# Performance work log

Hardware: AMD Instinct MI355X
Metric: run time of the kernel (lower is better)

The kernel has to match this reference:

```python
import jax, jax.numpy as jnp
import numpy as np

B, T, D, S = 64, 577, 768, 577  # batch, seq, hidden, v-out (=seq of e)


def setup_inputs() -> dict:
    key = jax.random.key(0)
    ks = jax.random.split(key, 8)
    sc = 1.0 / np.sqrt(D)
    return {
        "b": jax.random.normal(ks[0], (B, T, D), jnp.float32),
        "e": jax.random.normal(ks[1], (B, T, D), jnp.float32),
        "Wq": jax.random.normal(ks[2], (D, D), jnp.float32) * sc,
        "bq": jnp.zeros((D,), jnp.float32),
        "Wk": jax.random.normal(ks[3], (D, D), jnp.float32) * sc,
        "bk": jnp.zeros((D,), jnp.float32),
        "Wv": jax.random.normal(ks[4], (S, D), jnp.float32) * sc,
        "bv": jnp.zeros((S,), jnp.float32),
    }


def reference(b, e, Wq, bq, Wk, bk, Wv, bv):
    # Dropout layers are identity in eval mode.
    q = b @ Wq.T + bq                      # [B,T,D]
    k = e @ Wk.T + bk                      # [B,S,D]
    v = b @ Wv.T + bv                      # [B,T,S]
    # tanh(Q K^T) @ V^T : [B,T,S] @ [B,S,T] -> [B,T,T]
    attn = jnp.tanh(jnp.einsum("btd,bsd->bts", q, k))
    out = jnp.einsum("bts,bus->btu", attn, v)
    return out  # squeeze is a no-op for B>1
```

## Files before the change

### kernel.cpp

```cpp
#include <hip/hip_runtime.h>
#include <hip/hip_fp16.h>


typedef _Float16 f16x8 __attribute__((ext_vector_type(8)));
typedef _Float16 f16x4 __attribute__((ext_vector_type(4)));
typedef float f32x4 __attribute__((ext_vector_type(4)));

__global__ void cvt8_kernel(const float* __restrict__ src, _Float16* __restrict__ dst,
                            long long n8) {
    long long i = blockIdx.x * (long long)blockDim.x + threadIdx.x;
    const long long stride = gridDim.x * (long long)blockDim.x;
    for (; i < n8; i += stride) {
        const float4 f0 = ((const float4*)src)[2 * i];
        const float4 f1 = ((const float4*)src)[2 * i + 1];
        f16x8 h;
        h[0] = (_Float16)f0.x; h[1] = (_Float16)f0.y; h[2] = (_Float16)f0.z; h[3] = (_Float16)f0.w;
        h[4] = (_Float16)f1.x; h[5] = (_Float16)f1.y; h[6] = (_Float16)f1.z; h[7] = (_Float16)f1.w;
        ((f16x8*)dst)[i] = h;
    }
}

__global__ void cvtT_kernel(const float* __restrict__ src, _Float16* __restrict__ dst) {
    __shared__ float t[32][33];
    const int bx = blockIdx.x, by = blockIdx.y;
    const int tx = threadIdx.x & 31, ty = threadIdx.x >> 5;
#pragma unroll
    for (int k = 0; k < 4; ++k) {
        const int r = ty + 8 * k;
        t[r][tx] = src[(size_t)(by * 32 + r) * 768 + bx * 32 + tx];
    }
    __syncthreads();
#pragma unroll
    for (int k = 0; k < 4; ++k) {
        const int r = ty + 8 * k;
        dst[(size_t)(bx * 32 + r) * 768 + by * 32 + tx] = (_Float16)t[tx][r];
    }
}

__global__ void prep_kernel(const _Float16* __restrict__ WqT, const _Float16* __restrict__ WkT,
                            const float* __restrict__ bq, const float* __restrict__ bk,
                            float* __restrict__ w2f, _Float16* __restrict__ Mt_aug,
                            float* __restrict__ bias_aug) {
    const int wid = blockIdx.x * 4 + (threadIdx.x >> 6);
    const int lane = threadIdx.x & 63;
    if (wid < 768) {
        float s = 0.f;
        for (int k = 0; k < 12; ++k) s += (float)WqT[(size_t)wid * 768 + lane + 64 * k] * bk[lane + 64 * k];
        for (int o = 32; o; o >>= 1) s += __shfl_xor(s, o);
        if (lane == 0) Mt_aug[(size_t)768 * 768 + wid] = (_Float16)s;
    } else if (wid < 1536) {
        const int n = wid - 768;
        float s = 0.f;
        for (int k = 0; k < 12; ++k) s += (float)WkT[(size_t)n * 768 + lane + 64 * k] * bq[lane + 64 * k];
        for (int o = 32; o; o >>= 1) s += __shfl_xor(s, o);
        if (lane == 0) w2f[n] = s;
    } else if (wid == 1536) {
        float s = 0.f;
        for (int k = 0; k < 12; ++k) s += bq[lane + 64 * k] * bk[lane + 64 * k];
        for (int o = 32; o; o >>= 1) s += __shfl_xor(s, o);
        for (int k = 0; k < 12; ++k) bias_aug[lane + 64 * k] = 0.f;
        if (lane < 32) {
            float v = 0.f;
            if (lane == 0) v = s;
            if (lane == 1) v = 1.f;
            bias_aug[768 + lane] = v;
        }
    } else if (wid < 1568) {
        const int r = 769 + (wid - 1537);
        if (r < 800)
            for (int k = 0; k < 12; ++k) Mt_aug[(size_t)r * 768 + lane + 64 * k] = (_Float16)0.f;
    }
}

__global__ void cvt_e_aug_kernel(const float* __restrict__ e, const float* __restrict__ w2f,
                                 _Float16* __restrict__ dst, int rows) {
    const int wpb = blockDim.x >> 6;
    int wid = blockIdx.x * wpb + (threadIdx.x >> 6);
    const int nw = gridDim.x * wpb;
    const int lane = threadIdx.x & 63;
    for (int s = wid; s < rows; s += nw) {
        const float4* er = (const float4*)(e + (size_t)s * 768);
        _Float16* dr = dst + (size_t)s * 800;
        float dot = 0.f;
#pragma unroll
        for (int k = 0; k < 3; ++k) {
            const int idx = lane + 64 * k;
            const float4 v = er[idx];
            const float4 w = ((const float4*)w2f)[idx];
            dot += v.x * w.x + v.y * w.y + v.z * w.z + v.w * w.w;
            f16x4 h;
            h[0] = (_Float16)v.x; h[1] = (_Float16)v.y;
            h[2] = (_Float16)v.z; h[3] = (_Float16)v.w;
            *(f16x4*)(dr + 4 * idx) = h;
        }
        for (int o = 32; o; o >>= 1) dot += __shfl_xor(dot, o);
        if (lane < 32) {
            _Float16 v = (_Float16)0.f;
            if (lane == 0) v = (_Float16)1.f;
            if (lane == 1) v = (_Float16)dot;
            dr[768 + lane] = v;
        }
    }
}

__device__ __forceinline__ void gload16(const _Float16* g, _Float16* l) {
    __builtin_amdgcn_global_load_lds(
        (const __attribute__((address_space(1))) unsigned int*)(g),
        (__attribute__((address_space(3))) unsigned int*)(l),
        16, 0, 0);
}

template<bool TANH, bool OUT_F16, bool BIAS, int MODE>
__global__ __launch_bounds__(256)
void gemm_nt_f16(const _Float16* __restrict__ A, const _Float16* __restrict__ Bt,
                 const float* __restrict__ bias, void* __restrict__ Cp,
                 int M, int Nreal, int Nstore, int K,
                 int lda, int ldb, int ldc, int nTileN, int nTiles,
                 long long sA, long long sB, long long sC)
{
    __shared__ __align__(16) _Float16 lds[3 * 8192];

    int bid = blockIdx.x;
    int z, tm, tn;
    if (MODE == 0) {
        const int nwg = gridDim.x;
        const int q8 = nwg >> 3, r8 = nwg & 7;
        const int xcd = bid & 7, loc = bid >> 3;
        bid = (xcd < r8 ? xcd * (q8 + 1) : r8 * (q8 + 1) + (xcd - r8) * q8) + loc;
        z = 0;
        tm = bid / nTileN; tn = bid - tm * nTileN;
    } else {
        const int xcd = bid & 7, idx = bid >> 3;
        const int g = idx / nTiles, tile = idx - g * nTiles;
        z = g * 8 + xcd;
        tm = tile / nTileN; tn = tile - tm * nTileN;
    }
    const int m0 = tm << 7, n0 = tn << 7;

    const _Float16* Az = A + (size_t)z * sA;
    const _Float16* Bz = Bt + (size_t)z * sB;

    const int tid = threadIdx.x;
    const int lane = tid & 63;
    const int wid = tid >> 6;
    const int wm = wid >> 1, wn = wid & 1;

    const int r0 = tid >> 2;
    const int c0 = (((tid & 3) ^ ((tid >> 3) & 3)) << 3);
    const int rA0 = (m0 + r0      < M ? m0 + r0      : M - 1);
    const int rA1 = (m0 + r0 + 64 < M ? m0 + r0 + 64 : M - 1);
    const int rB0 = (n0 + r0      < Nreal ? n0 + r0      : Nreal - 1);
    const int rB1 = (n0 + r0 + 64 < Nreal ? n0 + r0 + 64 : Nreal - 1);
    const _Float16* pA0 = Az + (size_t)rA0 * lda + c0;
    const _Float16* pA1 = Az + (size_t)rA1 * lda + c0;
    const _Float16* pB0 = Bz + (size_t)rB0 * ldb + c0;
    const _Float16* pB1 = Bz + (size_t)rB1 * ldb + c0;

    const int o0 = tid * 8, o1 = (tid + 256) * 8;

    const int rr = lane & 15;
    const int hh = lane >> 4;
    const int sw = (rr >> 1) & 3;
    const int fAo = ((wm * 64 + rr) * 4 + (hh ^ sw)) * 8;
    const int fBo = ((wn * 64 + rr) * 4 + (hh ^ sw)) * 8;

    const f32x4 z4 = {0.f, 0.f, 0.f, 0.f};
    f32x4 acc[4][4];
#pragma unroll
    for (int i = 0; i < 4; ++i)
#pragma unroll
        for (int j = 0; j < 4; ++j) acc[i][j] = z4;

    const int nt = K >> 5;

#define STAGE(si, kt)                                              \
    do {                                                           \
        _Float16* base_ = lds + (si) * 8192;                       \
        const int ko_ = (kt) << 5;                                 \
        gload16(pA0 + ko_, base_ + o0);                            \
        gload16(pA1 + ko_, base_ + o1);                            \
        gload16(pB0 + ko_, base_ + 4096 + o0);                     \
        gload16(pB1 + ko_, base_ + 4096 + o1);                     \
    } while (0)

#define COMPUTE(si)                                                            \
    do {                                                                       \
        const _Float16* cA_ = lds + (si) * 8192;                               \
        const _Float16* cB_ = cA_ + 4096;                                      \
        f16x8 a_[4], b_[4];                                                    \
        _Pragma("unroll")                                                      \
        for (int mi = 0; mi < 4; ++mi) a_[mi] = *(const f16x8*)(cA_ + fAo + mi * 512); \
        _Pragma("unroll")                                                      \
        for (int ni = 0; ni < 4; ++ni) b_[ni] = *(const f16x8*)(cB_ + fBo + ni * 512); \
        _Pragma("unroll")                                                      \
        for (int mi = 0; mi < 4; ++mi)                                         \
            _Pragma("unroll")                                                  \
            for (int ni = 0; ni < 4; ++ni)                                     \
                acc[mi][ni] = __builtin_amdgcn_mfma_f32_16x16x32_f16(          \
                    a_[mi], b_[ni], acc[mi][ni], 0, 0, 0);                     \
    } while (0)

    STAGE(0, 0);
    STAGE(1, 1);

    for (int j = 0; j < nt - 1; ++j) {
        asm volatile("s_waitcnt vmcnt(4)" ::: "memory");
        __builtin_amdgcn_s_barrier();
        __builtin_amdgcn_sched_barrier(0);
        if (j + 2 < nt) STAGE((j + 2) % 3, j + 2);
        COMPUTE(j % 3);
    }
    asm volatile("s_waitcnt vmcnt(0)" ::: "memory");
    __builtin_amdgcn_s_barrier();
    __builtin_amdgcn_sched_barrier(0);
    COMPUTE((nt - 1) % 3);

#undef STAGE
#undef COMPUTE

    const int cr0 = (lane >> 4) << 2;
    const int cc = lane & 15;
    float*    Cf = (float*)Cp    + (size_t)z * sC;
    _Float16* Ch = (_Float16*)Cp + (size_t)z * sC;
#pragma unroll
    for (int mi = 0; mi < 4; ++mi) {
#pragma unroll
        for (int ni = 0; ni < 4; ++ni) {
            const int gc = n0 + wn * 64 + ni * 16 + cc;
            if (gc >= Nstore) continue;
            const bool real = gc < Nreal;
            float bb = 0.f;
            if (BIAS) bb = real ? bias[gc] : 0.f;
#pragma unroll
            for (int r = 0; r < 4; ++r) {
                const int gr = m0 + wm * 64 + mi * 16 + cr0 + r;
                if (gr >= M) continue;
                float x = real ? (acc[mi][ni][r] + bb) : 0.f;
                if (TANH) x = tanhf(x);
                if (OUT_F16) Ch[(size_t)gr * ldc + gc] = (_Float16)x;
                else         Cf[(size_t)gr * ldc + gc] = x;
            }
        }
    }
}

extern "C" void kernel_launch(void* const* d_in, const int* in_sizes, int n_in,
                              void* d_out, int out_size, void* d_ws, size_t ws_size,
                              hipStream_t stream)
{
    const float* b  = (const float*)d_in[0];
    const float* e  = (const float*)d_in[1];
    const float* Wq = (const float*)d_in[2];
    const float* bq = (const float*)d_in[3];
    const float* Wk = (const float*)d_in[4];
    const float* bk = (const float*)d_in[5];
    const float* Wv = (const float*)d_in[6];
    const float* bv = (const float*)d_in[7];
    float* out = (float*)d_out;

    const int BT = 36928, T = 577, S = 577, Sp = 608, Kb = 800;

    _Float16* WqT_h   = (_Float16*)d_ws;
    _Float16* WkT_h   = WqT_h + 589824;
    _Float16* Wv_h    = WkT_h + 589824;
    _Float16* Mt_aug  = Wv_h + 443136;
    float*    bias_aug = (float*)(Mt_aug + 614400);
    float*    w2f      = (float*)((_Float16*)bias_aug + 1600);
    _Float16* S1 = (_Float16*)w2f + 1536;
    _Float16* S2 = S1 + (size_t)BT * Kb;
    _Float16* S3 = S2 + (size_t)BT * Sp;
    _Float16* S4 = S3 + (size_t)BT * Kb;

    cvtT_kernel<<<dim3(24, 24), 256, 0, stream>>>(Wq, WqT_h);
    cvtT_kernel<<<dim3(24, 24), 256, 0, stream>>>(Wk, WkT_h);
    cvt8_kernel<<<217, 256, 0, stream>>>(Wv, Wv_h, 55392);
    prep_kernel<<<392, 256, 0, stream>>>(WqT_h, WkT_h, bq, bk, w2f, Mt_aug, bias_aug);
    gemm_nt_f16<false, true, false, 0><<<dim3(36, 1, 1), 256, 0, stream>>>(
        WkT_h, WqT_h, nullptr, Mt_aug, 768, 768, 768, 768, 768, 768, 768, 6, 0, 0, 0, 0);

    cvt8_kernel<<<2048, 256, 0, stream>>>(b, S1, 3545088);
    gemm_nt_f16<false, true, true, 0><<<dim3(1445, 1, 1), 256, 0, stream>>>(
        S1, Wv_h, bv, S2, BT, S, Sp, 768, 768, 768, Sp, 5, 0, 0, 0, 0);
    gemm_nt_f16<false, true, true, 0><<<dim3(2023, 1, 1), 256, 0, stream>>>(
        S1, Mt_aug, bias_aug, S3, BT, Kb, Kb, 768, 768, 768, Kb, 7, 0, 0, 0, 0);
    cvt_e_aug_kernel<<<2048, 256, 0, stream>>>(e, w2f, S1, BT);
    gemm_nt_f16<true, true, false, 1><<<dim3(1600, 1, 1), 256, 0, stream>>>(
        S3, S1, nullptr, S4, T, S, Sp, Kb, Kb, Kb, Sp, 5, 25,
        (long long)T * Kb, (long long)T * Kb, (long long)T * Sp);
    gemm_nt_f16<false, false, false, 1><<<dim3(1600, 1, 1), 256, 0, stream>>>(
        S4, S2, nullptr, out, T, T, T, Sp, Sp, Sp, T, 5, 25,
        (long long)T * Sp, (long long)T * Sp, (long long)T * T);
}
```

Before: 385.0 us.

## Merge Wv and Mt_aug projections into one wide GEMM over shared input

Places Wv_h directly after Mt_aug in the workspace so the two projection GEMMs on the converted b act as one GEMM with N=1377 (padded to 1408), writing a combined output buffer. Later GEMMs read their slices with a larger leading dimension. The two weight-transpose launches are also merged into one grid with a z dimension. This reads the b activation once instead of twice and removes kernel launches, at the cost of strided accesses in downstream GEMMs and an extra padded row region.

```diff
diff --git a/kernel.cpp b/kernel.cpp
--- a/kernel.cpp
+++ b/kernel.cpp
@@ -20,8 +20,11 @@
     }
 }
 
-__global__ void cvtT_kernel(const float* __restrict__ src, _Float16* __restrict__ dst) {
+__global__ void cvtT2_kernel(const float* __restrict__ s0, _Float16* __restrict__ d0,
+                             const float* __restrict__ s1, _Float16* __restrict__ d1) {
     __shared__ float t[32][33];
+    const float* src = blockIdx.z ? s1 : s0;
+    _Float16* dst = blockIdx.z ? d1 : d0;
     const int bx = blockIdx.x, by = blockIdx.y;
     const int tx = threadIdx.x & 31, ty = threadIdx.x >> 5;
 #pragma unroll
@@ -39,8 +42,9 @@
 
 __global__ void prep_kernel(const _Float16* __restrict__ WqT, const _Float16* __restrict__ WkT,
                             const float* __restrict__ bq, const float* __restrict__ bk,
+                            const float* __restrict__ bv,
                             float* __restrict__ w2f, _Float16* __restrict__ Mt_aug,
-                            float* __restrict__ bias_aug) {
+                            float* __restrict__ bias_mg) {
     const int wid = blockIdx.x * 4 + (threadIdx.x >> 6);
     const int lane = threadIdx.x & 63;
     if (wid < 768) {
@@ -58,17 +62,22 @@
         float s = 0.f;
         for (int k = 0; k < 12; ++k) s += bq[lane + 64 * k] * bk[lane + 64 * k];
         for (int o = 32; o; o >>= 1) s += __shfl_xor(s, o);
-        for (int k = 0; k < 12; ++k) bias_aug[lane + 64 * k] = 0.f;
         if (lane < 32) {
             float v = 0.f;
             if (lane == 0) v = s;
             if (lane == 1) v = 1.f;
-            bias_aug[768 + lane] = v;
-        }
-    } else if (wid < 1568) {
-        const int r = 769 + (wid - 1537);
-        if (r < 800)
-            for (int k = 0; k < 12; ++k) Mt_aug[(size_t)r * 768 + lane + 64 * k] = (_Float16)0.f;
+            bias_mg[768 + lane] = v;
+        }
+    } else if (wid < 1560) {
+        const int i = (wid - 1537) * 64 + lane;
+        if (i < 768) bias_mg[i] = 0.f;
+        else {
+            const int j = i + 32;
+            if (j < 1408) bias_mg[j] = (j < 1377) ? bv[j - 800] : 0.f;
+        }
+    } else if (wid < 1591) {
+        const int r = 769 + (wid - 1560);
+        for (int k = 0; k < 12; ++k) Mt_aug[(size_t)r * 768 + lane + 64 * k] = (_Float16)0.f;
     }
 }
 
@@ -259,35 +268,32 @@
     float* out = (float*)d_out;
 
     const int BT = 36928, T = 577, S = 577, Sp = 608, Kb = 800;
-
-    _Float16* WqT_h   = (_Float16*)d_ws;
-    _Float16* WkT_h   = WqT_h + 589824;
-    _Float16* Wv_h    = WkT_h + 589824;
-    _Float16* Mt_aug  = Wv_h + 443136;
-    float*    bias_aug = (float*)(Mt_aug + 614400);
-    float*    w2f      = (float*)((_Float16*)bias_aug + 1600);
-    _Float16* S1 = (_Float16*)w2f + 1536;
-    _Float16* S2 = S1 + (size_t)BT * Kb;
-    _Float16* S3 = S2 + (size_t)BT * Sp;
-    _Float16* S4 = S3 + (size_t)BT * Kb;
-
-    cvtT_kernel<<<dim3(24, 24), 256, 0, stream>>>(Wq, WqT_h);
-    cvtT_kernel<<<dim3(24, 24), 256, 0, stream>>>(Wk, WkT_h);
+    const int Nmg = 1408;
+
+    _Float16* WqT_h  = (_Float16*)d_ws;
+    _Float16* WkT_h  = WqT_h + 589824;
+    _Float16* Mt_aug = WkT_h + 589824;
+    _Float16* Wv_h   = Mt_aug + 614400;
+    float*    bias_mg = (float*)(Wv_h + 443136);
+    float*    w2f     = (float*)((_Float16*)bias_mg + 2816);
+    _Float16* S1    = (_Float16*)w2f + 1536;
+    _Float16* S_big = S1 + (size_t)BT * Kb;
+    _Float16* S4    = S_big + (size_t)BT * Nmg;
+
+    cvtT2_kernel<<<dim3(24, 24, 2), 256, 0, stream>>>(Wq, WqT_h, Wk, WkT_h);
     cvt8_kernel<<<217, 256, 0, stream>>>(Wv, Wv_h, 55392);
-    prep_kernel<<<392, 256, 0, stream>>>(WqT_h, WkT_h, bq, bk, w2f, Mt_aug, bias_aug);
+    prep_kernel<<<398, 256, 0, stream>>>(WqT_h, WkT_h, bq, bk, bv, w2f, Mt_aug, bias_mg);
     gemm_nt_f16<false, true, false, 0><<<dim3(36, 1, 1), 256, 0, stream>>>(
         WkT_h, WqT_h, nullptr, Mt_aug, 768, 768, 768, 768, 768, 768, 768, 6, 0, 0, 0, 0);
 
     cvt8_kernel<<<2048, 256, 0, stream>>>(b, S1, 3545088);
-    gemm_nt_f16<false, true, true, 0><<<dim3(1445, 1, 1), 256, 0, stream>>>(
-        S1, Wv_h, bv, S2, BT, S, Sp, 768, 768, 768, Sp, 5, 0, 0, 0, 0);
-    gemm_nt_f16<false, true, true, 0><<<dim3(2023, 1, 1), 256, 0, stream>>>(
-        S1, Mt_aug, bias_aug, S3, BT, Kb, Kb, 768, 768, 768, Kb, 7, 0, 0, 0, 0);
+    gemm_nt_f16<false, true, true, 0><<<dim3(3179, 1, 1), 256, 0, stream>>>(
+        S1, Mt_aug, bias_mg, S_big, BT, 1377, Nmg, 768, 768, 768, Nmg, 11, 0, 0, 0, 0);
     cvt_e_aug_kernel<<<2048, 256, 0, stream>>>(e, w2f, S1, BT);
     gemm_nt_f16<true, true, false, 1><<<dim3(1600, 1, 1), 256, 0, stream>>>(
-        S3, S1, nullptr, S4, T, S, Sp, Kb, Kb, Kb, Sp, 5, 25,
-        (long long)T * Kb, (long long)T * Kb, (long long)T * Sp);
+        S_big, S1, nullptr, S4, T, S, Sp, Kb, Nmg, Kb, Sp, 5, 25,
+        (long long)T * Nmg, (long long)T * Kb, (long long)T * Sp);
     gemm_nt_f16<false, false, false, 1><<<dim3(1600, 1, 1), 256, 0, stream>>>(
-        S4, S2, nullptr, out, T, T, T, Sp, Sp, Sp, T, 5, 25,
-        (long long)T * Sp, (long long)T * Sp, (long long)T * T);
-}
+        S4, S_big + 800, nullptr, out, T, T, T, Sp, Sp, Nmg, T, 5, 25,
+        (long long)T * Sp, (long long)T * Nmg, (long long)T * T);
+}
```

Measured after the change: 354.7 us. 1.09x faster.
